# Kernel tuning notes

Hardware: AMD Instinct MI355X
Metric: run time of the kernel (lower is better)

## Reference

```python
import jax, jax.numpy as jnp
import numpy as np

NEG_SLOPE = 0.2  # PyG GATConv default negative_slope
N_NODES = 50000


def gat_conv(x, src, dst, W, att_src, att_dst, bias, heads, out_ch):
    # x: [N, F_in]; src/dst: [E] (messages flow src -> dst, softmax over dst)
    N = x.shape[0]
    h = (x @ W).reshape(N, heads, out_ch)              # [N,H,C]
    a_src = jnp.sum(h * att_src, axis=-1)              # [N,H]
    a_dst = jnp.sum(h * att_dst, axis=-1)              # [N,H]
    e = jax.nn.leaky_relu(a_src[src] + a_dst[dst], NEG_SLOPE)   # [E,H]
    # numerically stable segment softmax over incoming edges of each dst node
    m = jax.ops.segment_max(e, dst, num_segments=N)    # [N,H]
    e = jnp.exp(e - m[dst])
    denom = jax.ops.segment_sum(e, dst, num_segments=N)
    alpha = e / (denom[dst] + 1e-16)                   # [E,H]
    msg = h[src] * alpha[:, :, None]                   # [E,H,C]
    out = jax.ops.segment_sum(msg, dst, num_segments=N)  # [N,H,C]
    return out.reshape(N, heads * out_ch) + bias


def add_self_loops(edge_index, num_nodes):
    loop = jnp.arange(num_nodes, dtype=edge_index.dtype)
    return jnp.concatenate([edge_index, jnp.stack([loop, loop])], axis=1)


def setup_inputs() -> dict:
    key = jax.random.key(0)
    ks = jax.random.split(key, 10)
    F_in, H, C, F_out = 256, 4, 64, 16
    x = jax.random.normal(ks[0], (N_NODES, F_in), dtype=jnp.float32)
    edge_index = jax.random.randint(ks[1], (2, 800000), 0, N_NODES, dtype=jnp.int64)
    s1 = 1.0 / np.sqrt(F_in)
    s2 = 1.0 / np.sqrt(H * C)
    return {
        "x": x,
        "edge_index": edge_index,
        "W1": jax.random.normal(ks[2], (F_in, H * C), dtype=jnp.float32) * s1,
        "att_src1": jax.random.normal(ks[3], (H, C), dtype=jnp.float32) * s2,
        "att_dst1": jax.random.normal(ks[4], (H, C), dtype=jnp.float32) * s2,
        "b1": jnp.zeros((H * C,), dtype=jnp.float32),
        "W2": jax.random.normal(ks[5], (H * C, F_out), dtype=jnp.float32) * s2,
        "att_src2": jax.random.normal(ks[6], (1, F_out), dtype=jnp.float32) * 0.25,
        "att_dst2": jax.random.normal(ks[7], (1, F_out), dtype=jnp.float32) * 0.25,
        "b2": jnp.zeros((F_out,), dtype=jnp.float32),
    }


def reference(x, edge_index, W1, att_src1, att_dst1, b1, W2, att_src2, att_dst2, b2):
    ei = add_self_loops(edge_index, x.shape[0])
    src, dst = ei[0], ei[1]
    H1, C1 = att_src1.shape
    h = gat_conv(x, src, dst, W1, att_src1, att_dst1, b1, H1, C1)
    h = jax.nn.relu(h)
    # F.dropout(training=False) is identity in eval mode
    H2, C2 = att_src2.shape
    out = gat_conv(h, src, dst, W2, att_src2, att_dst2, b2, H2, C2)
    return jax.nn.log_softmax(out, axis=1)
```

## Files before the change

### kernel.cpp

```cpp
#include <hip/hip_runtime.h>
#include <math.h>


typedef __attribute__((ext_vector_type(8))) short bf16x8;
typedef __attribute__((ext_vector_type(8))) unsigned short u16x8;
typedef __attribute__((ext_vector_type(4))) float f32x4;
typedef __attribute__((ext_vector_type(2))) float f32x2;

#define BCAP 1536

static __device__ inline unsigned short f2bf(float f) {
    unsigned u = __builtin_bit_cast(unsigned, f);
    unsigned r = (u + 0x7FFF + ((u >> 16) & 1)) >> 16;
    return (unsigned short)r;
}
static __device__ inline float bf2f(unsigned short u) {
    unsigned v = ((unsigned)u) << 16;
    return __builtin_bit_cast(float, v);
}
static __device__ inline float lrelu(float x) { return x > 0.f ? x : 0.2f * x; }

__global__ __launch_bounds__(256) void k_prep(const float* __restrict__ W1,
                                              const float* __restrict__ b1,
                                              short* __restrict__ w1t,
                                              float* __restrict__ b1p,
                                              int* __restrict__ fill_bkt,
                                              int nbuk) {
    int idx = blockIdx.x * 256 + threadIdx.x;
    if (idx < nbuk) fill_bkt[idx] = 0;
    if (idx < 256) {
        int ct = (idx >> 6) * 64 + (idx & 3) * 16 + ((idx & 63) >> 2);
        b1p[idx] = b1[ct];
    }
    int n = idx >> 8, k = idx & 255;
    w1t[n * 256 + k] = (short)f2bf(W1[k * 256 + n]);
}

__global__ __launch_bounds__(256) void k_bucketize(const int* __restrict__ ei,
                                                   int* __restrict__ fill_bkt,
                                                   uint2* __restrict__ tmp,
                                                   int E0, int nbuk) {
    __shared__ int hist[1024];
    __shared__ int base[1024];
    const int t = threadIdx.x;
    const int e0 = blockIdx.x * 4096;
    for (int b = t; b < nbuk; b += 256) hist[b] = 0;
    __syncthreads();
    int ss[16], ds[16];
    int nm = 0;
#pragma unroll
    for (int k = 0; k < 16; ++k) {
        int e = e0 + t + k * 256;
        if (e < E0) {
            ss[nm] = ei[e];
            ds[nm] = ei[E0 + e];
            atomicAdd(&hist[ds[nm] >> 6], 1);
            ++nm;
        }
    }
    __syncthreads();
    for (int b = t; b < nbuk; b += 256) {
        int c = hist[b];
        base[b] = c ? atomicAdd(&fill_bkt[b], c) : 0;
        hist[b] = 0;
    }
    __syncthreads();
    for (int k = 0; k < nm; ++k) {
        int b = ds[k] >> 6;
        int r = base[b] + atomicAdd(&hist[b], 1);
        if (r < BCAP) tmp[(long)b * BCAP + r] = make_uint2((unsigned)ss[k], (unsigned)ds[k]);
    }
}

__global__ __launch_bounds__(256) void k_csr_fill(const uint2* __restrict__ tmp,
                                                  const int* __restrict__ fill_bkt,
                                                  int* __restrict__ off,
                                                  int* __restrict__ csr,
                                                  int N, int nbuk) {
    __shared__ int hist[64];
    __shared__ int loff[64];
    __shared__ int lfill[64];
    __shared__ int sbase;
    const int b = blockIdx.x;
    const int t = threadIdx.x;
    if (t < 64) { hist[t] = 0; lfill[t] = 0; }
    __syncthreads();
    int cnt = min(fill_bkt[b], BCAP);
    const uint2* tp = tmp + (long)b * BCAP;
    for (int i = t; i < cnt; i += 256)
        atomicAdd(&hist[tp[i].y & 63], 1);
    if (t >= 64 && t < 128) {
        int l = t - 64;
        int acc = 0;
        for (int i = l; i < b; i += 64) acc += min(fill_bkt[i], BCAP);
#pragma unroll
        for (int o = 1; o < 64; o <<= 1) acc += __shfl_xor(acc, o);
        if (l == 0) sbase = acc + 64 * b;
        if (b == nbuk - 1 && l == 0) {
            int tot = acc + 64 * b + min(fill_bkt[b], BCAP) + (N - b * 64);
            off[N] = tot;
        }
    }
    __syncthreads();
    if (t < 64) {
        int v = hist[t] + 1;
        int incl = v;
#pragma unroll
        for (int o = 1; o < 64; o <<= 1) {
            int u = __shfl_up(incl, o);
            if (t >= (unsigned)o) incl += u;
        }
        int lo = sbase + incl - v;
        loff[t] = lo;
        int d = b * 64 + t;
        if (d < N) off[d] = lo;
    }
    __syncthreads();
    for (int i = t; i < cnt; i += 256) {
        uint2 e = tp[i];
        int dl = e.y & 63;
        int r = atomicAdd(&lfill[dl], 1);
        csr[loff[dl] + r] = (int)e.x;
    }
    __syncthreads();
    if (t < 64) {
        int d = b * 64 + t;
        if (d < N) csr[loff[t] + hist[t]] = d;
    }
}

__global__ __launch_bounds__(256) void k_gemm1_mfma(const float* __restrict__ A,
                                                    const short* __restrict__ Bt,
                                                    const float* __restrict__ att_s,
                                                    const float* __restrict__ att_d,
                                                    unsigned char* __restrict__ C8,
                                                    float* __restrict__ a1s,
                                                    float* __restrict__ a1d,
                                                    int M) {
    __shared__ short As[128][40];
    __shared__ short Bs[128][40];
    const int bm = blockIdx.y * 128;
    const int bn = blockIdx.x * 128;
    const int tid = threadIdx.x;
    const int lane = tid & 63;
    const int wave = tid >> 6;
    const int wm = (wave >> 1) * 64;
    const int wn = (wave & 1) * 64;
    const int l15 = lane & 15;
    const int l4 = lane >> 4;

    const int sr = tid >> 1;
    const int sh = (tid & 1) * 16;

    f32x4 acc[4][4] = {};

    for (int k0 = 0; k0 < 256; k0 += 32) {
        {
            float v[16];
            if (bm + sr < M) {
                const float* p = &A[(long)(bm + sr) * 256 + k0 + sh];
#pragma unroll
                for (int q = 0; q < 4; ++q) {
                    float4 fv = *(const float4*)(p + q * 4);
                    v[q * 4 + 0] = fv.x; v[q * 4 + 1] = fv.y;
                    v[q * 4 + 2] = fv.z; v[q * 4 + 3] = fv.w;
                }
            } else {
#pragma unroll
                for (int q = 0; q < 16; ++q) v[q] = 0.f;
            }
            short b[16];
#pragma unroll
            for (int q = 0; q < 16; ++q) b[q] = (short)f2bf(v[q]);
            *(bf16x8*)&As[sr][sh] = *(bf16x8*)&b[0];
            *(bf16x8*)&As[sr][sh + 8] = *(bf16x8*)&b[8];
        }
        {
            const short* p = &Bt[(long)(bn + sr) * 256 + k0 + sh];
            bf16x8 b0 = *(const bf16x8*)p;
            bf16x8 b1 = *(const bf16x8*)(p + 8);
            *(bf16x8*)&Bs[sr][sh] = b0;
            *(bf16x8*)&Bs[sr][sh + 8] = b1;
        }
        __syncthreads();

        bf16x8 af[4], bfr[4];
#pragma unroll
        for (int i = 0; i < 4; ++i)
            af[i] = *(const bf16x8*)&As[wm + i * 16 + l15][l4 * 8];
#pragma unroll
        for (int j = 0; j < 4; ++j)
            bfr[j] = *(const bf16x8*)&Bs[wn + j * 16 + l15][l4 * 8];
#pragma unroll
        for (int i = 0; i < 4; ++i)
#pragma unroll
            for (int j = 0; j < 4; ++j)
                acc[i][j] = __builtin_amdgcn_mfma_f32_16x16x32_bf16(af[i], bfr[j], acc[i][j], 0, 0, 0);
        __syncthreads();
    }

    const int h = (bn + wn) >> 6;
    float aws[4], awd[4];
#pragma unroll
    for (int j = 0; j < 4; ++j) {
        aws[j] = att_s[h * 64 + j * 16 + l15];
        awd[j] = att_d[h * 64 + j * 16 + l15];
    }

#pragma unroll
    for (int i = 0; i < 4; ++i) {
#pragma unroll
        for (int r = 0; r < 4; ++r) {
            float sv = 0.f, dv = 0.f;
#pragma unroll
            for (int j = 0; j < 4; ++j) {
                sv += acc[i][j][r] * aws[j];
                dv += acc[i][j][r] * awd[j];
            }
#pragma unroll
            for (int o = 1; o < 16; o <<= 1) {
                sv += __shfl_xor(sv, o);
                dv += __shfl_xor(dv, o);
            }
            int row = bm + wm + i * 16 + l4 * 4 + r;
            if (row < M) {
                if (l15 == 0) { a1s[row * 4 + h] = sv; a1d[row * 4 + h] = dv; }
                int d = 0;
                d = __builtin_amdgcn_cvt_pk_fp8_f32(acc[i][0][r], acc[i][1][r], d, false);
                d = __builtin_amdgcn_cvt_pk_fp8_f32(acc[i][2][r], acc[i][3][r], d, true);
                *(unsigned*)&C8[(long)row * 256 + (bn + wn) + l15 * 4] = (unsigned)d;
            }
        }
    }
}

__global__ __launch_bounds__(256) void k_gather1(const unsigned char* __restrict__ h1f8,
                                                 const int* __restrict__ off,
                                                 const int* __restrict__ csr,
                                                 const float* __restrict__ as1,
                                                 const float* __restrict__ ad1,
                                                 float* __restrict__ alphaE,
                                                 const float* __restrict__ b1p,
                                                 unsigned short* __restrict__ out1b,
                                                 int N) {
    int wid = blockIdx.x * 4 + (threadIdx.x >> 6);
    int lane = threadIdx.x & 63;
    if (wid >= N) return;
    int begin = off[wid], end = off[wid + 1];

    float4 ad4 = ((const float4*)ad1)[wid];
    float den0 = 0.f, den1 = 0.f, den2 = 0.f, den3 = 0.f;
    for (int j = begin + lane; j < end; j += 64) {
        int s = csr[j];
        float4 sc = ((const float4*)as1)[s];
        float e0 = __expf(lrelu(sc.x + ad4.x));
        float e1 = __expf(lrelu(sc.y + ad4.y));
        float e2 = __expf(lrelu(sc.z + ad4.z));
        float e3 = __expf(lrelu(sc.w + ad4.w));
        ((float4*)alphaE)[j] = make_float4(e0, e1, e2, e3);
        den0 += e0; den1 += e1; den2 += e2; den3 += e3;
    }
#pragma unroll
    for (int o = 32; o; o >>= 1) {
        den0 += __shfl_xor(den0, o);
        den1 += __shfl_xor(den1, o);
        den2 += __shfl_xor(den2, o);
        den3 += __shfl_xor(den3, o);
    }
    __threadfence_block();

    const int es = lane >> 4;
    const int cl = lane & 15;
    const int hc = cl >> 2;
    float denh = hc == 0 ? den0 : hc == 1 ? den1 : hc == 2 ? den2 : den3;
    const float inv_c = 1.f / (denh + 1e-16f);

    f32x2 acc2[8] = {};
#pragma unroll 2
    for (int j0 = begin; j0 < end; j0 += 4) {
        int j = j0 + es;
        bool valid = j < end;
        int jc = valid ? j : begin;
        int s = csr[jc];
        float a = valid ? alphaE[jc * 4 + hc] : 0.f;
        f32x2 av = {a, a};
        uint4 v = *(const uint4*)&h1f8[(long)s * 256 + cl * 16];
        unsigned w[4] = {v.x, v.y, v.z, v.w};
#pragma unroll
        for (int q = 0; q < 4; ++q) {
            f32x2 lo = __builtin_amdgcn_cvt_pk_f32_fp8((int)w[q], false);
            f32x2 hi = __builtin_amdgcn_cvt_pk_f32_fp8((int)w[q], true);
            acc2[q * 2 + 0] += av * lo;
            acc2[q * 2 + 1] += av * hi;
        }
    }
    float accf[16];
#pragma unroll
    for (int q = 0; q < 8; ++q) { accf[2 * q] = acc2[q].x; accf[2 * q + 1] = acc2[q].y; }
#pragma unroll
    for (int q = 0; q < 16; ++q) {
        accf[q] += __shfl_xor(accf[q], 16);
        accf[q] += __shfl_xor(accf[q], 32);
    }
    if (lane < 16) {
        unsigned pk[8];
#pragma unroll
        for (int q = 0; q < 8; ++q) {
            float v0 = fmaxf(accf[q * 2 + 0] * inv_c + b1p[cl * 16 + q * 2 + 0], 0.f);
            float v1 = fmaxf(accf[q * 2 + 1] * inv_c + b1p[cl * 16 + q * 2 + 1], 0.f);
            pk[q] = (unsigned)f2bf(v0) | ((unsigned)f2bf(v1) << 16);
        }
        unsigned short* dst = &out1b[(long)wid * 256 + cl * 16];
        *(uint4*)dst = make_uint4(pk[0], pk[1], pk[2], pk[3]);
        *(uint4*)(dst + 8) = make_uint4(pk[4], pk[5], pk[6], pk[7]);
    }
}

__global__ __launch_bounds__(256) void k_gemm2(const unsigned short* __restrict__ Xb,
                                               const float* __restrict__ W,
                                               const float* __restrict__ att_s,
                                               const float* __restrict__ att_d,
                                               float* __restrict__ h2,
                                               float* __restrict__ a2s,
                                               float* __restrict__ a2d, int N) {
    __shared__ float Ws[256 * 16];
    for (int i = threadIdx.x; i < 1024; i += 256)
        ((float4*)Ws)[i] = ((const float4*)W)[i];
    __syncthreads();
    int r = threadIdx.x >> 4, c = threadIdx.x & 15;
    int row = blockIdx.x * 16 + r;
    if (row >= N) return;
    const unsigned short* xr = Xb + (long)row * 256;
    float acc = 0.f;
    for (int k = 0; k < 256; k += 8) {
        u16x8 xv = *(const u16x8*)&xr[k];
        int kb = (k >> 6) * 64 + ((k & 63) >> 2);
#pragma unroll
        for (int q = 0; q < 8; ++q) {
            int ct = kb + (q & 3) * 16 + (q >> 2);
            acc += bf2f(xv[q]) * Ws[ct * 16 + c];
        }
    }
    h2[row * 16 + c] = acc;
    float vs = acc * att_s[c];
    float vd = acc * att_d[c];
    for (int o = 1; o < 16; o <<= 1) { vs += __shfl_xor(vs, o); vd += __shfl_xor(vd, o); }
    if (c == 0) { a2s[row] = vs; a2d[row] = vd; }
}

__global__ __launch_bounds__(256) void k_gather2(const float* __restrict__ h2,
                                                 const int* __restrict__ off,
                                                 const int* __restrict__ csr,
                                                 const float* __restrict__ a2s,
                                                 const float* __restrict__ a2d,
                                                 const float* __restrict__ b2,
                                                 float* __restrict__ out, int N) {
    int wid = blockIdx.x * 4 + (threadIdx.x >> 6);
    int lane = threadIdx.x & 63;
    if (wid >= N) return;
    int begin = off[wid], end = off[wid + 1];
    float adh = a2d[wid];
    float den = 0.f;
    for (int j = begin + lane; j < end; j += 64)
        den += __expf(lrelu(a2s[csr[j]] + adh));
#pragma unroll
    for (int o = 32; o; o >>= 1) den += __shfl_xor(den, o);
    float inv = 1.f / (den + 1e-16f);
    const int es = lane >> 4;
    const int c = lane & 15;
    float acc = 0.f;
#pragma unroll 2
    for (int j0 = begin; j0 < end; j0 += 4) {
        int j = j0 + es;
        bool valid = j < end;
        int jc = valid ? j : begin;
        int s = csr[jc];
        float a = valid ? __expf(lrelu(a2s[s] + adh)) : 0.f;
        acc += a * h2[(long)s * 16 + c];
    }
    acc += __shfl_xor(acc, 16);
    acc += __shfl_xor(acc, 32);
    float v = acc * inv + b2[c];
    float mx = v;
    for (int o = 1; o < 16; o <<= 1) mx = fmaxf(mx, __shfl_xor(mx, o));
    float se = __expf(v - mx);
    for (int o = 1; o < 16; o <<= 1) se += __shfl_xor(se, o);
    float r = v - mx - logf(se);
    if (lane < 16) out[(long)wid * 16 + c] = r;
}

extern "C" void kernel_launch(void* const* d_in, const int* in_sizes, int n_in,
                              void* d_out, int out_size, void* d_ws, size_t ws_size,
                              hipStream_t stream) {
    const float* x    = (const float*)d_in[0];
    const int*   ei   = (const int*)d_in[1];
    const float* W1   = (const float*)d_in[2];
    const float* as1w = (const float*)d_in[3];
    const float* ad1w = (const float*)d_in[4];
    const float* b1   = (const float*)d_in[5];
    const float* W2   = (const float*)d_in[6];
    const float* as2w = (const float*)d_in[7];
    const float* ad2w = (const float*)d_in[8];
    const float* b2   = (const float*)d_in[9];
    float* out = (float*)d_out;

    const int N    = in_sizes[0] / 256;
    const int E0   = in_sizes[1] / 2;
    const int Etot = E0 + N;
    const int NBUK = (N + 63) >> 6;

    char* p = (char*)d_ws;
    unsigned char*  h1f8  = (unsigned char*)p;  p += (size_t)N * 256;
    unsigned short* out1b = (unsigned short*)p; p += (size_t)N * 256 * sizeof(short);
    float* h2     = (float*)p; p += (size_t)N * 16 * sizeof(float);
    float* a1s    = (float*)p; p += (size_t)N * 4 * sizeof(float);
    float* a1d    = (float*)p; p += (size_t)N * 4 * sizeof(float);
    float* a2s    = (float*)p; p += (size_t)N * sizeof(float);
    float* a2d    = (float*)p; p += (size_t)N * sizeof(float);
    float* alphaE = (float*)p; p += (size_t)Etot * 4 * sizeof(float);
    float* b1p    = (float*)p; p += (size_t)256 * sizeof(float);
    int*   off    = (int*)p;   p += (size_t)(N + 1) * sizeof(int);
    int*   fillbk = (int*)p;   p += (size_t)NBUK * sizeof(int);
    short* w1t    = (short*)p; p += (size_t)256 * 256 * sizeof(short);
    int*   csr    = (int*)p;   p += (size_t)Etot * sizeof(int);
    uint2* tmp    = (uint2*)p; p += (size_t)NBUK * BCAP * sizeof(uint2);

    const int NW = (N + 3) / 4;

    hipLaunchKernelGGL(k_prep, dim3(256), dim3(256), 0, stream, W1, b1, w1t, b1p, fillbk, NBUK);

    hipLaunchKernelGGL(k_bucketize, dim3((E0 + 4095) / 4096), dim3(256), 0, stream,
                       ei, fillbk, tmp, E0, NBUK);
    hipLaunchKernelGGL(k_csr_fill, dim3(NBUK), dim3(256), 0, stream,
                       tmp, fillbk, off, csr, N, NBUK);

    hipLaunchKernelGGL(k_gemm1_mfma, dim3(2, (N + 127) / 128), dim3(256), 0, stream,
                       x, w1t, as1w, ad1w, h1f8, a1s, a1d, N);
    hipLaunchKernelGGL(k_gather1, dim3(NW), dim3(256), 0, stream,
                       h1f8, off, csr, a1s, a1d, alphaE, b1p, out1b, N);

    hipLaunchKernelGGL(k_gemm2, dim3((N + 15) / 16), dim3(256), 0, stream,
                       out1b, W2, as2w, ad2w, h2, a2s, a2d, N);
    hipLaunchKernelGGL(k_gather2, dim3(NW), dim3(256), 0, stream,
                       h2, off, csr, a2s, a2d, b2, out, N);
}
```

Before: 255.8 us.

## Fuse layer-1 attention exponent and denominator into CSR fill; widen GEMM K tile

The CSR fill kernel now runs after GEMM1 and computes each edge's exp-score and per-destination softmax denominators while it scatters edges. It writes alphaE and inverse denominators, so gather1 skips its separate scoring pass over incoming edges. GEMM1 also moves from a K step of 32 to 64, which halves the barrier and loop iterations at the cost of more shared memory and registers. The costs are shared-memory float atomics in csr_fill and the loss of overlap between csr_fill and the GEMM, since csr_fill must now wait for the GEMM's outputs.

```diff
diff --git a/kernel.cpp b/kernel.cpp
--- a/kernel.cpp
+++ b/kernel.cpp
@@ -72,63 +72,6 @@
     }
 }
 
-__global__ __launch_bounds__(256) void k_csr_fill(const uint2* __restrict__ tmp,
-                                                  const int* __restrict__ fill_bkt,
-                                                  int* __restrict__ off,
-                                                  int* __restrict__ csr,
-                                                  int N, int nbuk) {
-    __shared__ int hist[64];
-    __shared__ int loff[64];
-    __shared__ int lfill[64];
-    __shared__ int sbase;
-    const int b = blockIdx.x;
-    const int t = threadIdx.x;
-    if (t < 64) { hist[t] = 0; lfill[t] = 0; }
-    __syncthreads();
-    int cnt = min(fill_bkt[b], BCAP);
-    const uint2* tp = tmp + (long)b * BCAP;
-    for (int i = t; i < cnt; i += 256)
-        atomicAdd(&hist[tp[i].y & 63], 1);
-    if (t >= 64 && t < 128) {
-        int l = t - 64;
-        int acc = 0;
-        for (int i = l; i < b; i += 64) acc += min(fill_bkt[i], BCAP);
-#pragma unroll
-        for (int o = 1; o < 64; o <<= 1) acc += __shfl_xor(acc, o);
-        if (l == 0) sbase = acc + 64 * b;
-        if (b == nbuk - 1 && l == 0) {
-            int tot = acc + 64 * b + min(fill_bkt[b], BCAP) + (N - b * 64);
-            off[N] = tot;
-        }
-    }
-    __syncthreads();
-    if (t < 64) {
-        int v = hist[t] + 1;
-        int incl = v;
-#pragma unroll
-        for (int o = 1; o < 64; o <<= 1) {
-            int u = __shfl_up(incl, o);
-            if (t >= (unsigned)o) incl += u;
-        }
-        int lo = sbase + incl - v;
-        loff[t] = lo;
-        int d = b * 64 + t;
-        if (d < N) off[d] = lo;
-    }
-    __syncthreads();
-    for (int i = t; i < cnt; i += 256) {
-        uint2 e = tp[i];
-        int dl = e.y & 63;
-        int r = atomicAdd(&lfill[dl], 1);
-        csr[loff[dl] + r] = (int)e.x;
-    }
-    __syncthreads();
-    if (t < 64) {
-        int d = b * 64 + t;
-        if (d < N) csr[loff[t] + hist[t]] = d;
-    }
-}
-
 __global__ __launch_bounds__(256) void k_gemm1_mfma(const float* __restrict__ A,
                                                     const short* __restrict__ Bt,
                                                     const float* __restrict__ att_s,
@@ -137,8 +80,8 @@
                                                     float* __restrict__ a1s,
                                                     float* __restrict__ a1d,
                                                     int M) {
-    __shared__ short As[128][40];
-    __shared__ short Bs[128][40];
+    __shared__ short As[128][72];
+    __shared__ short Bs[128][72];
     const int bm = blockIdx.y * 128;
     const int bn = blockIdx.x * 128;
     const int tid = threadIdx.x;
@@ -150,52 +93,55 @@
     const int l4 = lane >> 4;
 
     const int sr = tid >> 1;
-    const int sh = (tid & 1) * 16;
+    const int sh = (tid & 1) * 32;
 
     f32x4 acc[4][4] = {};
 
-    for (int k0 = 0; k0 < 256; k0 += 32) {
+    for (int k0 = 0; k0 < 256; k0 += 64) {
         {
-            float v[16];
+            float v[32];
             if (bm + sr < M) {
                 const float* p = &A[(long)(bm + sr) * 256 + k0 + sh];
 #pragma unroll
-                for (int q = 0; q < 4; ++q) {
+                for (int q = 0; q < 8; ++q) {
                     float4 fv = *(const float4*)(p + q * 4);
                     v[q * 4 + 0] = fv.x; v[q * 4 + 1] = fv.y;
                     v[q * 4 + 2] = fv.z; v[q * 4 + 3] = fv.w;
                 }
             } else {
 #pragma unroll
-                for (int q = 0; q < 16; ++q) v[q] = 0.f;
+                for (int q = 0; q < 32; ++q) v[q] = 0.f;
             }
-            short b[16];
-#pragma unroll
-            for (int q = 0; q < 16; ++q) b[q] = (short)f2bf(v[q]);
-            *(bf16x8*)&As[sr][sh] = *(bf16x8*)&b[0];
-            *(bf16x8*)&As[sr][sh + 8] = *(bf16x8*)&b[8];
+            short b[32];
+#pragma unroll
+            for (int q = 0; q < 32; ++q) b[q] = (short)f2bf(v[q]);
+#pragma unroll
+            for (int q = 0; q < 4; ++q)
+                *(bf16x8*)&As[sr][sh + q * 8] = *(bf16x8*)&b[q * 8];
         }
         {
             const short* p = &Bt[(long)(bn + sr) * 256 + k0 + sh];
-            bf16x8 b0 = *(const bf16x8*)p;
-            bf16x8 b1 = *(const bf16x8*)(p + 8);
-            *(bf16x8*)&Bs[sr][sh] = b0;
-            *(bf16x8*)&Bs[sr][sh + 8] = b1;
+#pragma unroll
+            for (int q = 0; q < 4; ++q)
+                *(bf16x8*)&Bs[sr][sh + q * 8] = *(const bf16x8*)(p + q * 8);
         }
         __syncthreads();
 
-        bf16x8 af[4], bfr[4];
-#pragma unroll
-        for (int i = 0; i < 4; ++i)
-            af[i] = *(const bf16x8*)&As[wm + i * 16 + l15][l4 * 8];
-#pragma unroll
-        for (int j = 0; j < 4; ++j)
-            bfr[j] = *(const bf16x8*)&Bs[wn + j * 16 + l15][l4 * 8];
-#pragma unroll
-        for (int i = 0; i < 4; ++i)
+#pragma unroll
+        for (int kh = 0; kh < 2; ++kh) {
+            bf16x8 af[4], bfr[4];
+#pragma unroll
+            for (int i = 0; i < 4; ++i)
+                af[i] = *(const bf16x8*)&As[wm + i * 16 + l15][kh * 32 + l4 * 8];
 #pragma unroll
             for (int j = 0; j < 4; ++j)
-                acc[i][j] = __builtin_amdgcn_mfma_f32_16x16x32_bf16(af[i], bfr[j], acc[i][j], 0, 0, 0);
+                bfr[j] = *(const bf16x8*)&Bs[wn + j * 16 + l15][kh * 32 + l4 * 8];
+#pragma unroll
+            for (int i = 0; i < 4; ++i)
+#pragma unroll
+                for (int j = 0; j < 4; ++j)
+                    acc[i][j] = __builtin_amdgcn_mfma_f32_16x16x32_bf16(af[i], bfr[j], acc[i][j], 0, 0, 0);
+        }
         __syncthreads();
     }
 
@@ -234,12 +180,105 @@
     }
 }
 
+__global__ __launch_bounds__(256) void k_csr_fill(const uint2* __restrict__ tmp,
+                                                  const int* __restrict__ fill_bkt,
+                                                  const float* __restrict__ as1,
+                                                  const float* __restrict__ ad1,
+                                                  int* __restrict__ off,
+                                                  int* __restrict__ csr,
+                                                  float* __restrict__ alphaE,
+                                                  float* __restrict__ dinv,
+                                                  int N, int nbuk) {
+    __shared__ int hist[64];
+    __shared__ int loff[64];
+    __shared__ int lfill[64];
+    __shared__ float dens[64][4];
+    __shared__ int sbase;
+    const int b = blockIdx.x;
+    const int t = threadIdx.x;
+    if (t < 64) {
+        hist[t] = 0; lfill[t] = 0;
+        dens[t][0] = 0.f; dens[t][1] = 0.f; dens[t][2] = 0.f; dens[t][3] = 0.f;
+    }
+    __syncthreads();
+    int cnt = min(fill_bkt[b], BCAP);
+    const uint2* tp = tmp + (long)b * BCAP;
+    for (int i = t; i < cnt; i += 256)
+        atomicAdd(&hist[tp[i].y & 63], 1);
+    if (t >= 64 && t < 128) {
+        int l = t - 64;
+        int acc = 0;
+        for (int i = l; i < b; i += 64) acc += min(fill_bkt[i], BCAP);
+#pragma unroll
+        for (int o = 1; o < 64; o <<= 1) acc += __shfl_xor(acc, o);
+        if (l == 0) sbase = acc + 64 * b;
+        if (b == nbuk - 1 && l == 0) {
+            int tot = acc + 64 * b + min(fill_bkt[b], BCAP) + (N - b * 64);
+            off[N] = tot;
+        }
+    }
+    __syncthreads();
+    if (t < 64) {
+        int v = hist[t] + 1;
+        int incl = v;
+#pragma unroll
+        for (int o = 1; o < 64; o <<= 1) {
+            int u = __shfl_up(incl, o);
+            if (t >= (unsigned)o) incl += u;
+        }
+        int lo = sbase + incl - v;
+        loff[t] = lo;
+        int d = b * 64 + t;
+        if (d < N) off[d] = lo;
+    }
+    __syncthreads();
+    for (int i = t; i < cnt; i += 256) {
+        uint2 e = tp[i];
+        int dl = e.y & 63;
+        int s = (int)e.x;
+        int r = atomicAdd(&lfill[dl], 1);
+        int idx = loff[dl] + r;
+        csr[idx] = s;
+        float4 sc = ((const float4*)as1)[s];
+        float4 ad = ((const float4*)ad1)[(int)e.y];
+        float e0 = __expf(lrelu(sc.x + ad.x));
+        float e1 = __expf(lrelu(sc.y + ad.y));
+        float e2 = __expf(lrelu(sc.z + ad.z));
+        float e3 = __expf(lrelu(sc.w + ad.w));
+        ((float4*)alphaE)[idx] = make_float4(e0, e1, e2, e3);
+        atomicAdd(&dens[dl][0], e0);
+        atomicAdd(&dens[dl][1], e1);
+        atomicAdd(&dens[dl][2], e2);
+        atomicAdd(&dens[dl][3], e3);
+    }
+    __syncthreads();
+    if (t < 64) {
+        int d = b * 64 + t;
+        if (d < N) {
+            int idx = loff[t] + hist[t];
+            csr[idx] = d;
+            float4 sc = ((const float4*)as1)[d];
+            float4 ad = ((const float4*)ad1)[d];
+            float e0 = __expf(lrelu(sc.x + ad.x));
+            float e1 = __expf(lrelu(sc.y + ad.y));
+            float e2 = __expf(lrelu(sc.z + ad.z));
+            float e3 = __expf(lrelu(sc.w + ad.w));
+            ((float4*)alphaE)[idx] = make_float4(e0, e1, e2, e3);
+            float4 iv;
+            iv.x = 1.f / (dens[t][0] + e0 + 1e-16f);
+            iv.y = 1.f / (dens[t][1] + e1 + 1e-16f);
+            iv.z = 1.f / (dens[t][2] + e2 + 1e-16f);
+            iv.w = 1.f / (dens[t][3] + e3 + 1e-16f);
+            ((float4*)dinv)[d] = iv;
+        }
+    }
+}
+
 __global__ __launch_bounds__(256) void k_gather1(const unsigned char* __restrict__ h1f8,
                                                  const int* __restrict__ off,
                                                  const int* __restrict__ csr,
-                                                 const float* __restrict__ as1,
-                                                 const float* __restrict__ ad1,
-                                                 float* __restrict__ alphaE,
+                                                 const float* __restrict__ alphaE,
+                                                 const float* __restrict__ dinv,
                                                  const float* __restrict__ b1p,
                                                  unsigned short* __restrict__ out1b,
                                                  int N) {
@@ -247,33 +286,10 @@
     int lane = threadIdx.x & 63;
     if (wid >= N) return;
     int begin = off[wid], end = off[wid + 1];
-
-    float4 ad4 = ((const float4*)ad1)[wid];
-    float den0 = 0.f, den1 = 0.f, den2 = 0.f, den3 = 0.f;
-    for (int j = begin + lane; j < end; j += 64) {
-        int s = csr[j];
-        float4 sc = ((const float4*)as1)[s];
-        float e0 = __expf(lrelu(sc.x + ad4.x));
-        float e1 = __expf(lrelu(sc.y + ad4.y));
-        float e2 = __expf(lrelu(sc.z + ad4.z));
-        float e3 = __expf(lrelu(sc.w + ad4.w));
-        ((float4*)alphaE)[j] = make_float4(e0, e1, e2, e3);
-        den0 += e0; den1 += e1; den2 += e2; den3 += e3;
-    }
-#pragma unroll
-    for (int o = 32; o; o >>= 1) {
-        den0 += __shfl_xor(den0, o);
-        den1 += __shfl_xor(den1, o);
-        den2 += __shfl_xor(den2, o);
-        den3 += __shfl_xor(den3, o);
-    }
-    __threadfence_block();
-
     const int es = lane >> 4;
     const int cl = lane & 15;
     const int hc = cl >> 2;
-    float denh = hc == 0 ? den0 : hc == 1 ? den1 : hc == 2 ? den2 : den3;
-    const float inv_c = 1.f / (denh + 1e-16f);
+    const float inv_c = dinv[wid * 4 + hc];
 
     f32x2 acc2[8] = {};
 #pragma unroll 2
@@ -418,6 +434,7 @@
     float* a2s    = (float*)p; p += (size_t)N * sizeof(float);
     float* a2d    = (float*)p; p += (size_t)N * sizeof(float);
     float* alphaE = (float*)p; p += (size_t)Etot * 4 * sizeof(float);
+    float* dinv   = (float*)p; p += (size_t)N * 4 * sizeof(float);
     float* b1p    = (float*)p; p += (size_t)256 * sizeof(float);
     int*   off    = (int*)p;   p += (size_t)(N + 1) * sizeof(int);
     int*   fillbk = (int*)p;   p += (size_t)NBUK * sizeof(int);
@@ -431,13 +448,15 @@
 
     hipLaunchKernelGGL(k_bucketize, dim3((E0 + 4095) / 4096), dim3(256), 0, stream,
                        ei, fillbk, tmp, E0, NBUK);
-    hipLaunchKernelGGL(k_csr_fill, dim3(NBUK), dim3(256), 0, stream,
-                       tmp, fillbk, off, csr, N, NBUK);
 
     hipLaunchKernelGGL(k_gemm1_mfma, dim3(2, (N + 127) / 128), dim3(256), 0, stream,
                        x, w1t, as1w, ad1w, h1f8, a1s, a1d, N);
+
+    hipLaunchKernelGGL(k_csr_fill, dim3(NBUK), dim3(256), 0, stream,
+                       tmp, fillbk, a1s, a1d, off, csr, alphaE, dinv, N, NBUK);
+
     hipLaunchKernelGGL(k_gather1, dim3(NW), dim3(256), 0, stream,
-                       h1f8, off, csr, a1s, a1d, alphaE, b1p, out1b, N);
+                       h1f8, off, csr, alphaE, dinv, b1p, out1b, N);
 
     hipLaunchKernelGGL(k_gemm2, dim3((N + 15) / 16), dim3(256), 0, stream,
                        out1b, W2, as2w, ad2w, h2, a2s, a2d, N);
```

After: 269.9 us. 5.5% more time.

## Merge bucketize with GEMM1 and fuse GEMM2 into layer-1 gather

Applied to the files above, without the earlier changes.

Independent edge bucketization and the first GEMM now run in one launch, with blocks split by index, so the two can overlap on the device. The layer-2 projection (256x16 GEMM plus attention dot products) moves into the layer-1 gather epilogue. Each wave stages its output row in LDS and multiplies it by W2, which is preloaded in permuted layout. This removes the bf16 intermediate round-trip through global memory and two launches. In exchange, every gather block loads 16KB of W2 into LDS, which raises LDS use and may lower gather occupancy.

```diff
diff --git a/kernel.cpp b/kernel.cpp
--- a/kernel.cpp
+++ b/kernel.cpp
@@ -3,7 +3,6 @@
 
 
 typedef __attribute__((ext_vector_type(8))) short bf16x8;
-typedef __attribute__((ext_vector_type(8))) unsigned short u16x8;
 typedef __attribute__((ext_vector_type(4))) float f32x4;
 typedef __attribute__((ext_vector_type(2))) float f32x2;
 
@@ -14,16 +13,14 @@
     unsigned r = (u + 0x7FFF + ((u >> 16) & 1)) >> 16;
     return (unsigned short)r;
 }
-static __device__ inline float bf2f(unsigned short u) {
-    unsigned v = ((unsigned)u) << 16;
-    return __builtin_bit_cast(float, v);
-}
 static __device__ inline float lrelu(float x) { return x > 0.f ? x : 0.2f * x; }
 
 __global__ __launch_bounds__(256) void k_prep(const float* __restrict__ W1,
                                               const float* __restrict__ b1,
+                                              const float* __restrict__ W2,
                                               short* __restrict__ w1t,
                                               float* __restrict__ b1p,
+                                              float* __restrict__ w2p,
                                               int* __restrict__ fill_bkt,
                                               int nbuk) {
     int idx = blockIdx.x * 256 + threadIdx.x;
@@ -32,43 +29,153 @@
         int ct = (idx >> 6) * 64 + (idx & 3) * 16 + ((idx & 63) >> 2);
         b1p[idx] = b1[ct];
     }
+    if (idx < 4096) {
+        int p = idx >> 4, c = idx & 15;
+        int ct = (p >> 6) * 64 + (p & 3) * 16 + ((p & 63) >> 2);
+        w2p[idx] = W2[ct * 16 + c];
+    }
     int n = idx >> 8, k = idx & 255;
     w1t[n * 256 + k] = (short)f2bf(W1[k * 256 + n]);
 }
 
-__global__ __launch_bounds__(256) void k_bucketize(const int* __restrict__ ei,
-                                                   int* __restrict__ fill_bkt,
-                                                   uint2* __restrict__ tmp,
-                                                   int E0, int nbuk) {
-    __shared__ int hist[1024];
-    __shared__ int base[1024];
+__global__ __launch_bounds__(256) void k_buck_gemm1(
+        const int* __restrict__ ei, int* __restrict__ fill_bkt,
+        uint2* __restrict__ tmp, int E0, int nbuk,
+        const float* __restrict__ A, const short* __restrict__ Bt,
+        const float* __restrict__ att_s, const float* __restrict__ att_d,
+        unsigned char* __restrict__ C8,
+        float* __restrict__ a1s, float* __restrict__ a1d,
+        int M, int ngb) {
+    __shared__ __align__(16) char smem[20480];
     const int t = threadIdx.x;
-    const int e0 = blockIdx.x * 4096;
-    for (int b = t; b < nbuk; b += 256) hist[b] = 0;
-    __syncthreads();
-    int ss[16], ds[16];
-    int nm = 0;
-#pragma unroll
-    for (int k = 0; k < 16; ++k) {
-        int e = e0 + t + k * 256;
-        if (e < E0) {
-            ss[nm] = ei[e];
-            ds[nm] = ei[E0 + e];
-            atomicAdd(&hist[ds[nm] >> 6], 1);
-            ++nm;
-        }
-    }
-    __syncthreads();
-    for (int b = t; b < nbuk; b += 256) {
-        int c = hist[b];
-        base[b] = c ? atomicAdd(&fill_bkt[b], c) : 0;
-        hist[b] = 0;
-    }
-    __syncthreads();
-    for (int k = 0; k < nm; ++k) {
-        int b = ds[k] >> 6;
-        int r = base[b] + atomicAdd(&hist[b], 1);
-        if (r < BCAP) tmp[(long)b * BCAP + r] = make_uint2((unsigned)ss[k], (unsigned)ds[k]);
+
+    if ((int)blockIdx.x >= ngb) {
+        int* hist = (int*)smem;
+        int* base = (int*)(smem + 4096);
+        const int e0 = (blockIdx.x - ngb) * 4096;
+        for (int b = t; b < nbuk; b += 256) hist[b] = 0;
+        __syncthreads();
+        int ss[16], ds[16];
+        int nm = 0;
+#pragma unroll
+        for (int k = 0; k < 16; ++k) {
+            int e = e0 + t + k * 256;
+            if (e < E0) {
+                ss[nm] = ei[e];
+                ds[nm] = ei[E0 + e];
+                atomicAdd(&hist[ds[nm] >> 6], 1);
+                ++nm;
+            }
+        }
+        __syncthreads();
+        for (int b = t; b < nbuk; b += 256) {
+            int c = hist[b];
+            base[b] = c ? atomicAdd(&fill_bkt[b], c) : 0;
+            hist[b] = 0;
+        }
+        __syncthreads();
+        for (int k = 0; k < nm; ++k) {
+            int b = ds[k] >> 6;
+            int r = base[b] + atomicAdd(&hist[b], 1);
+            if (r < BCAP) tmp[(long)b * BCAP + r] = make_uint2((unsigned)ss[k], (unsigned)ds[k]);
+        }
+        return;
+    }
+
+    typedef short lds_row[40];
+    lds_row* As = (lds_row*)smem;
+    lds_row* Bs = (lds_row*)(smem + 10240);
+    const int bid = blockIdx.x;
+    const int bn = (bid & 1) * 128;
+    const int bm = (bid >> 1) * 128;
+    const int lane = t & 63;
+    const int wave = t >> 6;
+    const int wm = (wave >> 1) * 64;
+    const int wn = (wave & 1) * 64;
+    const int l15 = lane & 15;
+    const int l4 = lane >> 4;
+    const int sr = t >> 1;
+    const int sh = (t & 1) * 16;
+
+    f32x4 acc[4][4] = {};
+
+    for (int k0 = 0; k0 < 256; k0 += 32) {
+        {
+            float v[16];
+            if (bm + sr < M) {
+                const float* p = &A[(long)(bm + sr) * 256 + k0 + sh];
+#pragma unroll
+                for (int q = 0; q < 4; ++q) {
+                    float4 fv = *(const float4*)(p + q * 4);
+                    v[q * 4 + 0] = fv.x; v[q * 4 + 1] = fv.y;
+                    v[q * 4 + 2] = fv.z; v[q * 4 + 3] = fv.w;
+                }
+            } else {
+#pragma unroll
+                for (int q = 0; q < 16; ++q) v[q] = 0.f;
+            }
+            short b[16];
+#pragma unroll
+            for (int q = 0; q < 16; ++q) b[q] = (short)f2bf(v[q]);
+            *(bf16x8*)&As[sr][sh] = *(bf16x8*)&b[0];
+            *(bf16x8*)&As[sr][sh + 8] = *(bf16x8*)&b[8];
+        }
+        {
+            const short* p = &Bt[(long)(bn + sr) * 256 + k0 + sh];
+            bf16x8 b0 = *(const bf16x8*)p;
+            bf16x8 b1 = *(const bf16x8*)(p + 8);
+            *(bf16x8*)&Bs[sr][sh] = b0;
+            *(bf16x8*)&Bs[sr][sh + 8] = b1;
+        }
+        __syncthreads();
+
+        bf16x8 af[4], bfr[4];
+#pragma unroll
+        for (int i = 0; i < 4; ++i)
+            af[i] = *(const bf16x8*)&As[wm + i * 16 + l15][l4 * 8];
+#pragma unroll
+        for (int j = 0; j < 4; ++j)
+            bfr[j] = *(const bf16x8*)&Bs[wn + j * 16 + l15][l4 * 8];
+#pragma unroll
+        for (int i = 0; i < 4; ++i)
+#pragma unroll
+            for (int j = 0; j < 4; ++j)
+                acc[i][j] = __builtin_amdgcn_mfma_f32_16x16x32_bf16(af[i], bfr[j], acc[i][j], 0, 0, 0);
+        __syncthreads();
+    }
+
+    const int h = (bn + wn) >> 6;
+    float aws[4], awd[4];
+#pragma unroll
+    for (int j = 0; j < 4; ++j) {
+        aws[j] = att_s[h * 64 + j * 16 + l15];
+        awd[j] = att_d[h * 64 + j * 16 + l15];
+    }
+
+#pragma unroll
+    for (int i = 0; i < 4; ++i) {
+#pragma unroll
+        for (int r = 0; r < 4; ++r) {
+            float sv = 0.f, dv = 0.f;
+#pragma unroll
+            for (int j = 0; j < 4; ++j) {
+                sv += acc[i][j][r] * aws[j];
+                dv += acc[i][j][r] * awd[j];
+            }
+#pragma unroll
+            for (int o = 1; o < 16; o <<= 1) {
+                sv += __shfl_xor(sv, o);
+                dv += __shfl_xor(dv, o);
+            }
+            int row = bm + wm + i * 16 + l4 * 4 + r;
+            if (row < M) {
+                if (l15 == 0) { a1s[row * 4 + h] = sv; a1d[row * 4 + h] = dv; }
+                int d = 0;
+                d = __builtin_amdgcn_cvt_pk_fp8_f32(acc[i][0][r], acc[i][1][r], d, false);
+                d = __builtin_amdgcn_cvt_pk_fp8_f32(acc[i][2][r], acc[i][3][r], d, true);
+                *(unsigned*)&C8[(long)row * 256 + (bn + wn) + l15 * 4] = (unsigned)d;
+            }
+        }
     }
 }
 
@@ -129,111 +236,6 @@
     }
 }
 
-__global__ __launch_bounds__(256) void k_gemm1_mfma(const float* __restrict__ A,
-                                                    const short* __restrict__ Bt,
-                                                    const float* __restrict__ att_s,
-                                                    const float* __restrict__ att_d,
-                                                    unsigned char* __restrict__ C8,
-                                                    float* __restrict__ a1s,
-                                                    float* __restrict__ a1d,
-                                                    int M) {
-    __shared__ short As[128][40];
-    __shared__ short Bs[128][40];
-    const int bm = blockIdx.y * 128;
-    const int bn = blockIdx.x * 128;
-    const int tid = threadIdx.x;
-    const int lane = tid & 63;
-    const int wave = tid >> 6;
-    const int wm = (wave >> 1) * 64;
-    const int wn = (wave & 1) * 64;
-    const int l15 = lane & 15;
-    const int l4 = lane >> 4;
-
-    const int sr = tid >> 1;
-    const int sh = (tid & 1) * 16;
-
-    f32x4 acc[4][4] = {};
-
-    for (int k0 = 0; k0 < 256; k0 += 32) {
-        {
-            float v[16];
-            if (bm + sr < M) {
-                const float* p = &A[(long)(bm + sr) * 256 + k0 + sh];
-#pragma unroll
-                for (int q = 0; q < 4; ++q) {
-                    float4 fv = *(const float4*)(p + q * 4);
-                    v[q * 4 + 0] = fv.x; v[q * 4 + 1] = fv.y;
-                    v[q * 4 + 2] = fv.z; v[q * 4 + 3] = fv.w;
-                }
-            } else {
-#pragma unroll
-                for (int q = 0; q < 16; ++q) v[q] = 0.f;
-            }
-            short b[16];
-#pragma unroll
-            for (int q = 0; q < 16; ++q) b[q] = (short)f2bf(v[q]);
-            *(bf16x8*)&As[sr][sh] = *(bf16x8*)&b[0];
-            *(bf16x8*)&As[sr][sh + 8] = *(bf16x8*)&b[8];
-        }
-        {
-            const short* p = &Bt[(long)(bn + sr) * 256 + k0 + sh];
-            bf16x8 b0 = *(const bf16x8*)p;
-            bf16x8 b1 = *(const bf16x8*)(p + 8);
-            *(bf16x8*)&Bs[sr][sh] = b0;
-            *(bf16x8*)&Bs[sr][sh + 8] = b1;
-        }
-        __syncthreads();
-
-        bf16x8 af[4], bfr[4];
-#pragma unroll
-        for (int i = 0; i < 4; ++i)
-            af[i] = *(const bf16x8*)&As[wm + i * 16 + l15][l4 * 8];
-#pragma unroll
-        for (int j = 0; j < 4; ++j)
-            bfr[j] = *(const bf16x8*)&Bs[wn + j * 16 + l15][l4 * 8];
-#pragma unroll
-        for (int i = 0; i < 4; ++i)
-#pragma unroll
-            for (int j = 0; j < 4; ++j)
-                acc[i][j] = __builtin_amdgcn_mfma_f32_16x16x32_bf16(af[i], bfr[j], acc[i][j], 0, 0, 0);
-        __syncthreads();
-    }
-
-    const int h = (bn + wn) >> 6;
-    float aws[4], awd[4];
-#pragma unroll
-    for (int j = 0; j < 4; ++j) {
-        aws[j] = att_s[h * 64 + j * 16 + l15];
-        awd[j] = att_d[h * 64 + j * 16 + l15];
-    }
-
-#pragma unroll
-    for (int i = 0; i < 4; ++i) {
-#pragma unroll
-        for (int r = 0; r < 4; ++r) {
-            float sv = 0.f, dv = 0.f;
-#pragma unroll
-            for (int j = 0; j < 4; ++j) {
-                sv += acc[i][j][r] * aws[j];
-                dv += acc[i][j][r] * awd[j];
-            }
-#pragma unroll
-            for (int o = 1; o < 16; o <<= 1) {
-                sv += __shfl_xor(sv, o);
-                dv += __shfl_xor(dv, o);
-            }
-            int row = bm + wm + i * 16 + l4 * 4 + r;
-            if (row < M) {
-                if (l15 == 0) { a1s[row * 4 + h] = sv; a1d[row * 4 + h] = dv; }
-                int d = 0;
-                d = __builtin_amdgcn_cvt_pk_fp8_f32(acc[i][0][r], acc[i][1][r], d, false);
-                d = __builtin_amdgcn_cvt_pk_fp8_f32(acc[i][2][r], acc[i][3][r], d, true);
-                *(unsigned*)&C8[(long)row * 256 + (bn + wn) + l15 * 4] = (unsigned)d;
-            }
-        }
-    }
-}
-
 __global__ __launch_bounds__(256) void k_gather1(const unsigned char* __restrict__ h1f8,
                                                  const int* __restrict__ off,
                                                  const int* __restrict__ csr,
@@ -241,111 +243,117 @@
                                                  const float* __restrict__ ad1,
                                                  float* __restrict__ alphaE,
                                                  const float* __restrict__ b1p,
-                                                 unsigned short* __restrict__ out1b,
+                                                 const float* __restrict__ w2p,
+                                                 const float* __restrict__ as2w,
+                                                 const float* __restrict__ ad2w,
+                                                 float* __restrict__ h2,
+                                                 float* __restrict__ a2s,
+                                                 float* __restrict__ a2d,
                                                  int N) {
-    int wid = blockIdx.x * 4 + (threadIdx.x >> 6);
-    int lane = threadIdx.x & 63;
-    if (wid >= N) return;
-    int begin = off[wid], end = off[wid + 1];
-
-    float4 ad4 = ((const float4*)ad1)[wid];
-    float den0 = 0.f, den1 = 0.f, den2 = 0.f, den3 = 0.f;
-    for (int j = begin + lane; j < end; j += 64) {
-        int s = csr[j];
-        float4 sc = ((const float4*)as1)[s];
-        float e0 = __expf(lrelu(sc.x + ad4.x));
-        float e1 = __expf(lrelu(sc.y + ad4.y));
-        float e2 = __expf(lrelu(sc.z + ad4.z));
-        float e3 = __expf(lrelu(sc.w + ad4.w));
-        ((float4*)alphaE)[j] = make_float4(e0, e1, e2, e3);
-        den0 += e0; den1 += e1; den2 += e2; den3 += e3;
-    }
-#pragma unroll
-    for (int o = 32; o; o >>= 1) {
-        den0 += __shfl_xor(den0, o);
-        den1 += __shfl_xor(den1, o);
-        den2 += __shfl_xor(den2, o);
-        den3 += __shfl_xor(den3, o);
-    }
-    __threadfence_block();
-
-    const int es = lane >> 4;
-    const int cl = lane & 15;
-    const int hc = cl >> 2;
-    float denh = hc == 0 ? den0 : hc == 1 ? den1 : hc == 2 ? den2 : den3;
-    const float inv_c = 1.f / (denh + 1e-16f);
-
-    f32x2 acc2[8] = {};
+    __shared__ float Ws[4096];
+    __shared__ float sw[4][256];
+    const int t = threadIdx.x;
+    for (int i = t; i < 1024; i += 256)
+        ((float4*)Ws)[i] = ((const float4*)w2p)[i];
+    __syncthreads();
+
+    int wid = blockIdx.x * 4 + (t >> 6);
+    int lane = t & 63;
+    const int w = t >> 6;
+    if (wid < N) {
+        int begin = off[wid], end = off[wid + 1];
+
+        float4 ad4 = ((const float4*)ad1)[wid];
+        float den0 = 0.f, den1 = 0.f, den2 = 0.f, den3 = 0.f;
+        for (int j = begin + lane; j < end; j += 64) {
+            int s = csr[j];
+            float4 sc = ((const float4*)as1)[s];
+            float e0 = __expf(lrelu(sc.x + ad4.x));
+            float e1 = __expf(lrelu(sc.y + ad4.y));
+            float e2 = __expf(lrelu(sc.z + ad4.z));
+            float e3 = __expf(lrelu(sc.w + ad4.w));
+            ((float4*)alphaE)[j] = make_float4(e0, e1, e2, e3);
+            den0 += e0; den1 += e1; den2 += e2; den3 += e3;
+        }
+#pragma unroll
+        for (int o = 32; o; o >>= 1) {
+            den0 += __shfl_xor(den0, o);
+            den1 += __shfl_xor(den1, o);
+            den2 += __shfl_xor(den2, o);
+            den3 += __shfl_xor(den3, o);
+        }
+        __threadfence_block();
+
+        const int es = lane >> 4;
+        const int cl = lane & 15;
+        const int hc = cl >> 2;
+        float denh = hc == 0 ? den0 : hc == 1 ? den1 : hc == 2 ? den2 : den3;
+        const float inv_c = 1.f / (denh + 1e-16f);
+
+        f32x2 acc2[8] = {};
 #pragma unroll 2
-    for (int j0 = begin; j0 < end; j0 += 4) {
-        int j = j0 + es;
-        bool valid = j < end;
-        int jc = valid ? j : begin;
-        int s = csr[jc];
-        float a = valid ? alphaE[jc * 4 + hc] : 0.f;
-        f32x2 av = {a, a};
-        uint4 v = *(const uint4*)&h1f8[(long)s * 256 + cl * 16];
-        unsigned w[4] = {v.x, v.y, v.z, v.w};
-#pragma unroll
-        for (int q = 0; q < 4; ++q) {
-            f32x2 lo = __builtin_amdgcn_cvt_pk_f32_fp8((int)w[q], false);
-            f32x2 hi = __builtin_amdgcn_cvt_pk_f32_fp8((int)w[q], true);
-            acc2[q * 2 + 0] += av * lo;
-            acc2[q * 2 + 1] += av * hi;
-        }
-    }
-    float accf[16];
-#pragma unroll
-    for (int q = 0; q < 8; ++q) { accf[2 * q] = acc2[q].x; accf[2 * q + 1] = acc2[q].y; }
-#pragma unroll
-    for (int q = 0; q < 16; ++q) {
-        accf[q] += __shfl_xor(accf[q], 16);
-        accf[q] += __shfl_xor(accf[q], 32);
-    }
-    if (lane < 16) {
-        unsigned pk[8];
-#pragma unroll
-        for (int q = 0; q < 8; ++q) {
-            float v0 = fmaxf(accf[q * 2 + 0] * inv_c + b1p[cl * 16 + q * 2 + 0], 0.f);
-            float v1 = fmaxf(accf[q * 2 + 1] * inv_c + b1p[cl * 16 + q * 2 + 1], 0.f);
-            pk[q] = (unsigned)f2bf(v0) | ((unsigned)f2bf(v1) << 16);
-        }
-        unsigned short* dst = &out1b[(long)wid * 256 + cl * 16];
-        *(uint4*)dst = make_uint4(pk[0], pk[1], pk[2], pk[3]);
-        *(uint4*)(dst + 8) = make_uint4(pk[4], pk[5], pk[6], pk[7]);
-    }
-}
-
-__global__ __launch_bounds__(256) void k_gemm2(const unsigned short* __restrict__ Xb,
-                                               const float* __restrict__ W,
-                                               const float* __restrict__ att_s,
-                                               const float* __restrict__ att_d,
-                                               float* __restrict__ h2,
-                                               float* __restrict__ a2s,
-                                               float* __restrict__ a2d, int N) {
-    __shared__ float Ws[256 * 16];
-    for (int i = threadIdx.x; i < 1024; i += 256)
-        ((float4*)Ws)[i] = ((const float4*)W)[i];
-    __syncthreads();
-    int r = threadIdx.x >> 4, c = threadIdx.x & 15;
-    int row = blockIdx.x * 16 + r;
-    if (row >= N) return;
-    const unsigned short* xr = Xb + (long)row * 256;
-    float acc = 0.f;
-    for (int k = 0; k < 256; k += 8) {
-        u16x8 xv = *(const u16x8*)&xr[k];
-        int kb = (k >> 6) * 64 + ((k & 63) >> 2);
-#pragma unroll
-        for (int q = 0; q < 8; ++q) {
-            int ct = kb + (q & 3) * 16 + (q >> 2);
-            acc += bf2f(xv[q]) * Ws[ct * 16 + c];
-        }
-    }
-    h2[row * 16 + c] = acc;
-    float vs = acc * att_s[c];
-    float vd = acc * att_d[c];
-    for (int o = 1; o < 16; o <<= 1) { vs += __shfl_xor(vs, o); vd += __shfl_xor(vd, o); }
-    if (c == 0) { a2s[row] = vs; a2d[row] = vd; }
+        for (int j0 = begin; j0 < end; j0 += 4) {
+            int j = j0 + es;
+            bool valid = j < end;
+            int jc = valid ? j : begin;
+            int s = csr[jc];
+            float a = valid ? alphaE[jc * 4 + hc] : 0.f;
+            f32x2 av = {a, a};
+            uint4 v = *(const uint4*)&h1f8[(long)s * 256 + cl * 16];
+            unsigned wd[4] = {v.x, v.y, v.z, v.w};
+#pragma unroll
+            for (int q = 0; q < 4; ++q) {
+                f32x2 lo = __builtin_amdgcn_cvt_pk_f32_fp8((int)wd[q], false);
+                f32x2 hi = __builtin_amdgcn_cvt_pk_f32_fp8((int)wd[q], true);
+                acc2[q * 2 + 0] += av * lo;
+                acc2[q * 2 + 1] += av * hi;
+            }
+        }
+        float accf[16];
+#pragma unroll
+        for (int q = 0; q < 8; ++q) { accf[2 * q] = acc2[q].x; accf[2 * q + 1] = acc2[q].y; }
+#pragma unroll
+        for (int q = 0; q < 16; ++q) {
+            accf[q] += __shfl_xor(accf[q], 16);
+            accf[q] += __shfl_xor(accf[q], 32);
+        }
+        float v[16];
+#pragma unroll
+        for (int q = 0; q < 16; ++q)
+            v[q] = fmaxf(accf[q] * inv_c + b1p[cl * 16 + q], 0.f);
+        if (es == 0) {
+#pragma unroll
+            for (int q4 = 0; q4 < 4; ++q4)
+                *(float4*)&sw[w][cl * 16 + q4 * 4] =
+                    make_float4(v[q4 * 4 + 0], v[q4 * 4 + 1], v[q4 * 4 + 2], v[q4 * 4 + 3]);
+        }
+        __threadfence_block();
+
+        const int c = cl;
+        const int kq = es;
+        float hacc = 0.f;
+        const float* swr = sw[w];
+#pragma unroll
+        for (int p0 = 0; p0 < 64; p0 += 4) {
+            int p = kq * 64 + p0;
+            float4 xv = *(const float4*)&swr[p];
+            hacc += xv.x * Ws[(p + 0) * 16 + c];
+            hacc += xv.y * Ws[(p + 1) * 16 + c];
+            hacc += xv.z * Ws[(p + 2) * 16 + c];
+            hacc += xv.w * Ws[(p + 3) * 16 + c];
+        }
+        hacc += __shfl_xor(hacc, 16);
+        hacc += __shfl_xor(hacc, 32);
+        if (lane < 16) h2[(long)wid * 16 + c] = hacc;
+        float vs = hacc * as2w[c];
+        float vd = hacc * ad2w[c];
+#pragma unroll
+        for (int o = 1; o < 16; o <<= 1) {
+            vs += __shfl_xor(vs, o);
+            vd += __shfl_xor(vd, o);
+        }
+        if (lane == 0) { a2s[wid] = vs; a2d[wid] = vd; }
+    }
 }
 
 __global__ __launch_bounds__(256) void k_gather2(const float* __restrict__ h2,
@@ -408,10 +416,11 @@
     const int E0   = in_sizes[1] / 2;
     const int Etot = E0 + N;
     const int NBUK = (N + 63) >> 6;
+    const int NGB  = 2 * ((N + 127) / 128);
+    const int NBB  = (E0 + 4095) / 4096;
 
     char* p = (char*)d_ws;
-    unsigned char*  h1f8  = (unsigned char*)p;  p += (size_t)N * 256;
-    unsigned short* out1b = (unsigned short*)p; p += (size_t)N * 256 * sizeof(short);
+    unsigned char* h1f8 = (unsigned char*)p; p += (size_t)N * 256;
     float* h2     = (float*)p; p += (size_t)N * 16 * sizeof(float);
     float* a1s    = (float*)p; p += (size_t)N * 4 * sizeof(float);
     float* a1d    = (float*)p; p += (size_t)N * 4 * sizeof(float);
@@ -419,6 +428,7 @@
     float* a2d    = (float*)p; p += (size_t)N * sizeof(float);
     float* alphaE = (float*)p; p += (size_t)Etot * 4 * sizeof(float);
     float* b1p    = (float*)p; p += (size_t)256 * sizeof(float);
+    float* w2p    = (float*)p; p += (size_t)4096 * sizeof(float);
     int*   off    = (int*)p;   p += (size_t)(N + 1) * sizeof(int);
     int*   fillbk = (int*)p;   p += (size_t)NBUK * sizeof(int);
     short* w1t    = (short*)p; p += (size_t)256 * 256 * sizeof(short);
@@ -427,20 +437,20 @@
 
     const int NW = (N + 3) / 4;
 
-    hipLaunchKernelGGL(k_prep, dim3(256), dim3(256), 0, stream, W1, b1, w1t, b1p, fillbk, NBUK);
-
-    hipLaunchKernelGGL(k_bucketize, dim3((E0 + 4095) / 4096), dim3(256), 0, stream,
-                       ei, fillbk, tmp, E0, NBUK);
+    hipLaunchKernelGGL(k_prep, dim3(256), dim3(256), 0, stream,
+                       W1, b1, W2, w1t, b1p, w2p, fillbk, NBUK);
+
+    hipLaunchKernelGGL(k_buck_gemm1, dim3(NGB + NBB), dim3(256), 0, stream,
+                       ei, fillbk, tmp, E0, NBUK,
+                       x, w1t, as1w, ad1w, h1f8, a1s, a1d, N, NGB);
+
     hipLaunchKernelGGL(k_csr_fill, dim3(NBUK), dim3(256), 0, stream,
                        tmp, fillbk, off, csr, N, NBUK);
 
-    hipLaunchKernelGGL(k_gemm1_mfma, dim3(2, (N + 127) / 128), dim3(256), 0, stream,
-                       x, w1t, as1w, ad1w, h1f8, a1s, a1d, N);
     hipLaunchKernelGGL(k_gather1, dim3(NW), dim3(256), 0, stream,
-                       h1f8, off, csr, a1s, a1d, alphaE, b1p, out1b, N);
-
-    hipLaunchKernelGGL(k_gemm2, dim3((N + 15) / 16), dim3(256), 0, stream,
-                       out1b, W2, as2w, ad2w, h2, a2s, a2d, N);
+                       h1f8, off, csr, a1s, a1d, alphaE, b1p, w2p,
+                       as2w, ad2w, h2, a2s, a2d, N);
+
     hipLaunchKernelGGL(k_gather2, dim3(NW), dim3(256), 0, stream,
                        h2, off, csr, a2s, a2d, b2, out, N);
 }
```

Measured after the change: 265.4 us. 1.04x slower.
